# Kernel optimization log

Measured on AMD Instinct MI355X. Metric: run time of the kernel, lower is better.

## Reference

```python
import jax, jax.numpy as jnp
import numpy as np

N = 100000      # nodes
E = 1600000     # edges (before self-loops)
D = 14          # node_dim
H = 64          # hidden_dim
HEADS = 2
C = H // HEADS  # per-head channels = 32
NEG_SLOPE = 0.2 # GATv2Conv default


def setup_inputs() -> dict:
    key = jax.random.key(0)
    ks = jax.random.split(key, 32)
    p = lambda k, shape, s=0.05: (jax.random.normal(k, shape, jnp.float32) * s)
    inp = {
        'node_features': jax.random.normal(ks[0], (N, D), jnp.float32),
        'edge_index': jax.random.randint(ks[1], (2, E), 0, N, jnp.int32),
        # node_proj
        'proj_W': p(ks[2], (D, H)), 'proj_b': p(ks[3], (H,)),
        # GATv2 layer 1 (W_l for source msgs, W_r for target query)
        'g1_Wl': p(ks[4], (H, H)), 'g1_Wr': p(ks[5], (H, H)),
        'g1_att': p(ks[6], (HEADS, C)), 'g1_b': p(ks[7], (H,)),
        # GATv2 layer 2
        'g2_Wl': p(ks[8], (H, H)), 'g2_Wr': p(ks[9], (H, H)),
        'g2_att': p(ks[10], (HEADS, C)), 'g2_b': p(ks[11], (H,)),
        # LayerNorms
        'ln1_g': jnp.ones((H,), jnp.float32), 'ln1_b': jnp.zeros((H,), jnp.float32),
        'ln2_g': jnp.ones((H,), jnp.float32), 'ln2_b': jnp.zeros((H,), jnp.float32),
        # GRU (single step, h0=0). Gate order r,z,n like torch.
        'gru_Wi': p(ks[12], (H, 3 * H)), 'gru_Wh': p(ks[13], (H, 3 * H)),
        'gru_bi': p(ks[14], (3 * H,)), 'gru_bh': p(ks[15], (3 * H,)),
        # heads
        'hu_W': p(ks[16], (H, 1)), 'hu_b': p(ks[17], (1,)),
        'hf_W': p(ks[18], (H, 1)), 'hf_b': p(ks[19], (1,)),
        'ho_W': p(ks[20], (H, 1)), 'ho_b': p(ks[21], (1,)),
        'hc_W': p(ks[22], (H, 1)), 'hc_b': p(ks[23], (1,)),
    }
    return inp


def _layer_norm(x, g, b, eps=1e-5):
    mu = jnp.mean(x, axis=-1, keepdims=True)
    var = jnp.var(x, axis=-1, keepdims=True)
    return (x - mu) * jax.lax.rsqrt(var + eps) * g + b


def _gatv2(x, src, dst, Wl, Wr, att, b):
    n = x.shape[0]
    xl = (x @ Wl).reshape(n, HEADS, C)   # source messages
    xr = (x @ Wr).reshape(n, HEADS, C)   # target queries
    e = jax.nn.leaky_relu(xl[src] + xr[dst], NEG_SLOPE)       # [E', HEADS, C]
    s = jnp.einsum('ehc,hc->eh', e, att)                       # [E', HEADS]
    m = jax.ops.segment_max(s, dst, num_segments=n)            # segment softmax
    ex = jnp.exp(s - m[dst])
    den = jax.ops.segment_sum(ex, dst, num_segments=n)
    alpha = ex / (den[dst] + 1e-16)
    out = jax.ops.segment_sum(alpha[:, :, None] * xl[src], dst, num_segments=n)
    return out.reshape(n, H) + b


def reference(node_features, edge_index, proj_W, proj_b,
              g1_Wl, g1_Wr, g1_att, g1_b,
              g2_Wl, g2_Wr, g2_att, g2_b,
              ln1_g, ln1_b, ln2_g, ln2_b,
              gru_Wi, gru_Wh, gru_bi, gru_bh,
              hu_W, hu_b, hf_W, hf_b, ho_W, ho_b, hc_W, hc_b):
    n = node_features.shape[0]
    # add self-loops (PyG GATv2Conv default)
    loops = jnp.arange(n, dtype=edge_index.dtype)
    src = jnp.concatenate([edge_index[0], loops])
    dst = jnp.concatenate([edge_index[1], loops])

    x = node_features @ proj_W + proj_b
    x = jax.nn.elu(_gatv2(x, src, dst, g1_Wl, g1_Wr, g1_att, g1_b))
    x = _layer_norm(x, ln1_g, ln1_b)
    x = jax.nn.elu(_gatv2(x, src, dst, g2_Wl, g2_Wr, g2_att, g2_b))
    x = _layer_norm(x, ln2_g, ln2_b)

    # single-step GRU, h0 = 0 (gate order r, z, n as in torch)
    gi = x @ gru_Wi + gru_bi
    gi_r, gi_z, gi_n = jnp.split(gi, 3, axis=-1)
    bh_r, bh_z, bh_n = jnp.split(gru_bh, 3)
    r = jax.nn.sigmoid(gi_r + bh_r)
    z = jax.nn.sigmoid(gi_z + bh_z)
    nn_ = jnp.tanh(gi_n + r * bh_n)
    x = (1.0 - z) * nn_  # h' = (1-z)*n + z*h0, h0=0

    utilisation = jax.nn.sigmoid(x @ hu_W + hu_b)
    feasibility = jax.nn.sigmoid(x @ hf_W + hf_b)
    overtime = jax.nn.relu(x @ ho_W + ho_b)
    confidence = jax.nn.sigmoid(x @ hc_W + hc_b)
    return (utilisation, feasibility, overtime, confidence)
```

## Files before the change

### kernel.cpp

```cpp
#include <hip/hip_runtime.h>

#define NDIM 14
#define HDIM 64
#define NB 512
#define EPB 16
#define GSTR 72

typedef __attribute__((ext_vector_type(8))) _Float16 half8;
typedef __attribute__((ext_vector_type(2))) __fp16 fp16x2;
typedef __attribute__((ext_vector_type(4))) float f32x4;

static __device__ __forceinline__ float sigmoidf_(float x) { return 1.f / (1.f + __expf(-x)); }
static __device__ __forceinline__ float lrelu_(float x) { return x > 0.f ? x : 0.2f * x; }

static __device__ __forceinline__ float readlane_f(float x, int lane) {
  return __int_as_float(__builtin_amdgcn_readlane(__float_as_int(x), lane));
}

template <int CTRL>
static __device__ __forceinline__ float dpp_add_f(float x) {
  int v = __builtin_amdgcn_update_dpp(0, __float_as_int(x), CTRL, 0xF, 0xF, true);
  return x + __int_as_float(v);
}

static __device__ __forceinline__ float reduce16(float p) {
  p = dpp_add_f<0xB1>(p);
  p = dpp_add_f<0x4E>(p);
  p = dpp_add_f<0x141>(p);
  p = dpp_add_f<0x140>(p);
  return p;
}
static __device__ __forceinline__ float head_reduce32(float p) {
  p = reduce16(p);
  p += __int_as_float(__builtin_amdgcn_ds_swizzle(__float_as_int(p), 0x401F));
  return p;
}
static __device__ __forceinline__ float full_reduce64(float p) {
  p = head_reduce32(p);
  p += __shfl_xor(p, 32, 64);
  return p;
}

static __device__ __forceinline__ unsigned pk_add(unsigned a, unsigned b) {
  unsigned d; asm("v_pk_add_f16 %0, %1, %2" : "=v"(d) : "v"(a), "v"(b)); return d;
}
static __device__ __forceinline__ unsigned pk_mul(unsigned a, unsigned b) {
  unsigned d; asm("v_pk_mul_f16 %0, %1, %2" : "=v"(d) : "v"(a), "v"(b)); return d;
}
static __device__ __forceinline__ unsigned pk_max(unsigned a, unsigned b) {
  unsigned d; asm("v_pk_max_f16 %0, %1, %2" : "=v"(d) : "v"(a), "v"(b)); return d;
}
static __device__ __forceinline__ unsigned cvt_pk_u(float a, float b) {
  fp16x2 h = __builtin_amdgcn_cvt_pkrtz(a, b);
  unsigned u; __builtin_memcpy(&u, &h, 4); return u;
}
static __device__ __forceinline__ fp16x2 as_h2(unsigned u) {
  fp16x2 h; __builtin_memcpy(&h, &u, 4); return h;
}
static __device__ __forceinline__ float cvt_lo(unsigned u) {
  float r; asm("v_cvt_f32_f16 %0, %1" : "=v"(r) : "v"(u)); return r;
}
template <int CTRL>
static __device__ __forceinline__ unsigned pk_dpp_add(unsigned x) {
  unsigned v = (unsigned)__builtin_amdgcn_update_dpp(0, (int)x, CTRL, 0xF, 0xF, true);
  return pk_add(x, v);
}
static __device__ __forceinline__ unsigned pk_reduce32(unsigned p) {
  p = pk_dpp_add<0xB1>(p);
  p = pk_dpp_add<0x4E>(p);
  p = pk_dpp_add<0x141>(p);
  p = pk_dpp_add<0x140>(p);
  p = pk_add(p, (unsigned)__builtin_amdgcn_ds_swizzle((int)p, 0x401F));
  return p;
}

__global__ void __launch_bounds__(256) k_bin(const int* __restrict__ ei,
                      unsigned* __restrict__ pairs, int* __restrict__ bucket_cur,
                      int E, int bsh) {
  __shared__ int h[NB];
  __shared__ int gb[NB];
  int t = threadIdx.x;
  for (int i = t; i < NB; i += 256) h[i] = 0;
  __syncthreads();
  int c0 = blockIdx.x * (256 * EPB);
  unsigned pr[EPB];
  int br[EPB];
  unsigned lmask = (1u << bsh) - 1u;
#pragma unroll
  for (int i = 0; i < EPB; ++i) {
    int e = c0 + t + i * 256;
    if (e < E) {
      int s = ei[e], d = ei[E + e];
      int b = d >> bsh;
      int r = atomicAdd(&h[b], 1);
      pr[i] = (((unsigned)d & lmask) << 17) | (unsigned)s;
      br[i] = b | (r << 9);
    } else br[i] = -1;
  }
  __syncthreads();
  for (int i = t; i < NB; i += 256)
    if (h[i]) gb[i] = atomicAdd(&bucket_cur[i], h[i]);
  __syncthreads();
#pragma unroll
  for (int i = 0; i < EPB; ++i) {
    if (br[i] >= 0) pairs[gb[br[i] & (NB - 1)] + (br[i] >> 9)] = pr[i];
  }
}

__global__ void __launch_bounds__(256) k_csr(const unsigned* __restrict__ pairs,
                      const int* __restrict__ bcur_final, int* __restrict__ row_off,
                      int* __restrict__ deg, int* __restrict__ csr_src,
                      int N, int bsh, int cap) {
  __shared__ int h[1024];
  __shared__ int cu[1024];
  __shared__ int wtot[4];
  int b = blockIdx.x;
  int node0 = b << bsh;
  int range = 1 << bsh;
  int nr = N - node0; if (nr > range) nr = range;
  if (nr <= 0) return;
  int e0 = b * cap, e1 = bcur_final[b];
  int tid = threadIdx.x;
  for (int i = tid; i < range; i += 256) h[i] = 0;
  __syncthreads();
  for (int e = e0 + tid; e < e1; e += 256)
    atomicAdd(&h[pairs[e] >> 17], 1);
  __syncthreads();
  if (range == 256) {
    int lane = tid & 63, wid = tid >> 6;
    int v = (tid < nr) ? h[tid] : 0;
    int x = v;
#pragma unroll
    for (int m = 1; m <= 32; m <<= 1) {
      int t2 = __shfl_up(x, m, 64);
      if (lane >= m) x += t2;
    }
    if (lane == 63) wtot[wid] = x;
    __syncthreads();
    int woff = 0;
#pragma unroll
    for (int w = 0; w < 4; ++w) woff += (w < wid) ? wtot[w] : 0;
    int excl = woff + x - v;
    if (tid < nr) {
      row_off[node0 + tid] = e0 + excl;
      deg[node0 + tid] = v;
      cu[tid] = excl;
    }
  } else {
    if (tid == 0) {
      int acc = 0;
      for (int i = 0; i < nr; ++i) {
        row_off[node0 + i] = e0 + acc;
        deg[node0 + i] = h[i];
        cu[i] = acc;
        acc += h[i];
      }
    }
  }
  __syncthreads();
  for (int e = e0 + tid; e < e1; e += 256) {
    unsigned pk = pairs[e];
    int dl = (int)(pk >> 17);
    int s = (int)(pk & 0x1FFFFu);
    int p = atomicAdd(&cu[dl], 1);
    csr_src[e0 + p] = s;
  }
}

__global__ void k_wprep(const float* __restrict__ projW, const float* __restrict__ projB,
                        const float* __restrict__ Wl1, const float* __restrict__ Wr1,
                        const float* __restrict__ Wi, const float* __restrict__ Wl2,
                        const float* __restrict__ Wr2,
                        float* __restrict__ Wfl, float* __restrict__ Wfr,
                        float* __restrict__ bfl, float* __restrict__ bfr,
                        _Float16* __restrict__ Wt, _Float16* __restrict__ Wb,
                        int* __restrict__ bcur, int cap) {
  int blk = blockIdx.x;
  if (blk < 4) {
    int t = blk * 256 + threadIdx.x;
    int total = (NDIM + 1) * HDIM;
    if (t >= total) return;
    int r = t / HDIM, c = t % HDIM;
    float al = 0.f, ar = 0.f;
    if (r < NDIM) {
      for (int k = 0; k < HDIM; ++k) {
        float w = projW[r * HDIM + k];
        al += w * Wl1[k * HDIM + c];
        ar += w * Wr1[k * HDIM + c];
      }
      Wfl[r * HDIM + c] = al;
      Wfr[r * HDIM + c] = ar;
    } else {
      for (int k = 0; k < HDIM; ++k) {
        float w = projB[k];
        al += w * Wl1[k * HDIM + c];
        ar += w * Wr1[k * HDIM + c];
      }
      bfl[c] = al;
      bfr[c] = ar;
    }
  } else if (blk < 52) {
    int t = (blk - 4) * 256 + threadIdx.x;
    if (t >= 192 * 64) return;
    int col = t / 64, row = t % 64;
    Wt[col * GSTR + row] = (_Float16)Wi[row * 192 + col];
  } else if (blk < 84) {
    int t = (blk - 52) * 256 + threadIdx.x;
    if (t >= 128 * 64) return;
    int col = t >> 6, row = t & 63;
    float v = (col < 64) ? Wl2[row * 64 + col] : Wr2[row * 64 + (col - 64)];
    Wb[col * GSTR + row] = (_Float16)v;
  } else {
    int i = (blk - 84) * 256 + threadIdx.x;
    if (i < NB) bcur[i] = i * cap;
  }
}

__global__ void k1_xlxr(const float* __restrict__ nf, const float* __restrict__ Wfl,
                        const float* __restrict__ Wfr, const float* __restrict__ bfl,
                        const float* __restrict__ bfr, _Float16* __restrict__ XL16,
                        _Float16* __restrict__ XR16, int N) {
  int n = blockIdx.x * (blockDim.x >> 6) + (threadIdx.x >> 6);
  int j = threadIdx.x & 63;
  if (n >= N) return;
  float nfv = (j < NDIM) ? nf[n * NDIM + j] : 0.f;
  float al = bfl[j], ar = bfr[j];
#pragma unroll
  for (int k = 0; k < NDIM; ++k) {
    float xk = readlane_f(nfv, k);
    al += xk * Wfl[k * HDIM + j];
    ar += xk * Wfr[k * HDIM + j];
  }
  XL16[n * HDIM + j] = (_Float16)al;
  XR16[n * HDIM + j] = (_Float16)ar;
}

__global__ void k_agg(const int* __restrict__ csr_src, const int* __restrict__ row_off,
                      const int* __restrict__ deg, const _Float16* __restrict__ XL16,
                      const _Float16* __restrict__ XR16, const float* __restrict__ att,
                      const float* __restrict__ gb, const float* __restrict__ lng,
                      const float* __restrict__ lnb, float* __restrict__ Y, int N) {
  int n = blockIdx.x * (blockDim.x >> 6) + (threadIdx.x >> 6);
  int j = threadIdx.x & 63;
  if (n >= N) return;
  float xr = (float)XR16[(size_t)n * HDIM + j];
  float attv = att[j];
  unsigned xr_pk  = cvt_pk_u(xr, xr);
  unsigned att_pk = cvt_pk_u(attv, attv);
  unsigned c02_pk = 0x32663266u;
  fp16x2 one_pk = as_h2(0x3C003C00u);
  const unsigned short* XLu = (const unsigned short*)XL16;
  unsigned ju = (unsigned)j;

  float xl = (float)XL16[(size_t)n * HDIM + j];
  float p = head_reduce32(lrelu_(xl + xr) * attv);
  float ex = __expf(p);
  float acc0 = ex * xl, acc1 = 0.f;
  float den0 = ex, den1 = 0.f;

  int base = row_off[n], cnt = deg[n];
  for (int c0 = 0; c0 < cnt; c0 += 64) {
    int m_ = cnt - c0; if (m_ > 64) m_ = 64;
    int sidx = (j < m_) ? csr_src[base + c0 + j] : 0;
    int npairs = m_ >> 1;
    int pp = 0;
    for (; pp + 8 <= npairs; pp += 8) {
      unsigned x[8];
#pragma unroll
      for (int u = 0; u < 8; ++u) {
        int sa = __builtin_amdgcn_readlane(sidx, 2 * (pp + u));
        int sb = __builtin_amdgcn_readlane(sidx, 2 * (pp + u) + 1);
        unsigned ua = XLu[((unsigned)sa << 6) + ju];
        unsigned ub = XLu[((unsigned)sb << 6) + ju];
        x[u] = __builtin_amdgcn_perm(ub, ua, 0x05040100u);
      }
#pragma unroll
      for (int u = 0; u < 8; ++u) {
        unsigned t = pk_add(x[u], xr_pk);
        unsigned lr = pk_max(t, pk_mul(t, c02_pk));
        unsigned sc = pk_mul(lr, att_pk);
        sc = pk_reduce32(sc);
        float s_a = cvt_lo(sc), s_b = cvt_lo(sc >> 16);
        float e_a = __expf(s_a), e_b = __expf(s_b);
        fp16x2 exk = __builtin_amdgcn_cvt_pkrtz(e_a, e_b);
        if (u & 1) {
          acc1 = __builtin_amdgcn_fdot2(as_h2(x[u]), exk, acc1, false);
          den1 = __builtin_amdgcn_fdot2(exk, one_pk, den1, false);
        } else {
          acc0 = __builtin_amdgcn_fdot2(as_h2(x[u]), exk, acc0, false);
          den0 = __builtin_amdgcn_fdot2(exk, one_pk, den0, false);
        }
      }
    }
    for (; pp < npairs; ++pp) {
      int sa = __builtin_amdgcn_readlane(sidx, 2 * pp);
      int sb = __builtin_amdgcn_readlane(sidx, 2 * pp + 1);
      unsigned ua = XLu[((unsigned)sa << 6) + ju];
      unsigned ub = XLu[((unsigned)sb << 6) + ju];
      unsigned xu = __builtin_amdgcn_perm(ub, ua, 0x05040100u);
      unsigned t = pk_add(xu, xr_pk);
      unsigned lr = pk_max(t, pk_mul(t, c02_pk));
      unsigned sc = pk_mul(lr, att_pk);
      sc = pk_reduce32(sc);
      float s_a = cvt_lo(sc), s_b = cvt_lo(sc >> 16);
      float e_a = __expf(s_a), e_b = __expf(s_b);
      fp16x2 exk = __builtin_amdgcn_cvt_pkrtz(e_a, e_b);
      acc0 = __builtin_amdgcn_fdot2(as_h2(xu), exk, acc0, false);
      den0 = __builtin_amdgcn_fdot2(exk, one_pk, den0, false);
    }
    if (m_ & 1) {
      int s = __builtin_amdgcn_readlane(sidx, m_ - 1);
      float xls = (float)XL16[(size_t)s * HDIM + j];
      float pq = head_reduce32(lrelu_(xls + xr) * attv);
      float ee = __expf(pq);
      acc0 += ee * xls;
      den0 += ee;
    }
  }

  float acc = acc0 + acc1;
  float den = den0 + den1;
  float y = acc / (den + 1e-16f) + gb[j];
  y = y > 0.f ? y : __expf(y) - 1.f;
  float mu = full_reduce64(y) * (1.f / 64.f);
  float d = y - mu;
  float var = full_reduce64(d * d) * (1.f / 64.f);
  Y[n * HDIM + j] = d * rsqrtf(var + 1e-5f) * lng[j] + lnb[j];
}

__global__ void __launch_bounds__(256) k3_mfma(const float* __restrict__ Y,
                      const _Float16* __restrict__ Wb, _Float16* __restrict__ XL16,
                      _Float16* __restrict__ XR16, int N) {
  __shared__ _Float16 W[128 * GSTR];
  for (int i = threadIdx.x; i < 128 * GSTR / 8; i += 256)
    ((int4*)W)[i] = ((const int4*)Wb)[i];
  __syncthreads();
  int wave = blockIdx.x * 4 + (threadIdx.x >> 6);
  int nwaves = gridDim.x * 4;
  int lane = threadIdx.x & 63;
  int c = lane & 15, q = lane >> 4;
  for (int n0 = wave * 16; n0 < N; n0 += nwaves * 16) {
    bool okrow = (n0 + c) < N;
    const float* yrow = Y + (size_t)(n0 + c) * HDIM + q * 8;
    float4 v0 = {0,0,0,0}, v1 = {0,0,0,0}, v2 = {0,0,0,0}, v3 = {0,0,0,0};
    if (okrow) {
      v0 = *(const float4*)(yrow);
      v1 = *(const float4*)(yrow + 4);
      v2 = *(const float4*)(yrow + 32);
      v3 = *(const float4*)(yrow + 36);
    }
    half8 a0, a1;
    a0[0]=(_Float16)v0.x; a0[1]=(_Float16)v0.y; a0[2]=(_Float16)v0.z; a0[3]=(_Float16)v0.w;
    a0[4]=(_Float16)v1.x; a0[5]=(_Float16)v1.y; a0[6]=(_Float16)v1.z; a0[7]=(_Float16)v1.w;
    a1[0]=(_Float16)v2.x; a1[1]=(_Float16)v2.y; a1[2]=(_Float16)v2.z; a1[3]=(_Float16)v2.w;
    a1[4]=(_Float16)v3.x; a1[5]=(_Float16)v3.y; a1[6]=(_Float16)v3.z; a1[7]=(_Float16)v3.w;

    f32x4 acc[8];
#pragma unroll
    for (int t = 0; t < 8; ++t) acc[t] = (f32x4){0.f, 0.f, 0.f, 0.f};
#pragma unroll
    for (int t = 0; t < 8; ++t) {
      half8 b0 = *(const half8*)(&W[(t * 16 + c) * GSTR + q * 8]);
      half8 b1 = *(const half8*)(&W[(t * 16 + c) * GSTR + 32 + q * 8]);
      acc[t] = __builtin_amdgcn_mfma_f32_16x16x32_f16(a0, b0, acc[t], 0, 0, 0);
      acc[t] = __builtin_amdgcn_mfma_f32_16x16x32_f16(a1, b1, acc[t], 0, 0, 0);
    }
#pragma unroll
    for (int t = 0; t < 4; ++t) {
#pragma unroll
      for (int i = 0; i < 4; ++i) {
        int n = n0 + q * 4 + i;
        if (n < N) {
          XL16[(size_t)n * HDIM + t * 16 + c] = (_Float16)acc[t][i];
          XR16[(size_t)n * HDIM + t * 16 + c] = (_Float16)acc[t + 4][i];
        }
      }
    }
  }
}

__global__ void __launch_bounds__(256) k5_gru_mfma(const float* __restrict__ Y,
                       const _Float16* __restrict__ Wt,
                       const float* __restrict__ bi, const float* __restrict__ bh,
                       const float* __restrict__ huW, const float* __restrict__ hub,
                       const float* __restrict__ hfW, const float* __restrict__ hfb,
                       const float* __restrict__ hoW, const float* __restrict__ hob,
                       const float* __restrict__ hcW, const float* __restrict__ hcb,
                       float* __restrict__ out, int N) {
  __shared__ _Float16 W[192 * GSTR];
  __shared__ float BS[192];
  __shared__ float BHN[64];
  for (int i = threadIdx.x; i < 192 * GSTR / 8; i += 256)
    ((int4*)W)[i] = ((const int4*)Wt)[i];
  for (int i = threadIdx.x; i < 192; i += 256) BS[i] = bi[i] + (i < 128 ? bh[i] : 0.f);
  for (int i = threadIdx.x; i < 64; i += 256) BHN[i] = bh[128 + i];
  __syncthreads();

  int wave = blockIdx.x * 4 + (threadIdx.x >> 6);
  int nwaves = gridDim.x * 4;
  int lane = threadIdx.x & 63;
  int c = lane & 15, q = lane >> 4;

  float hu_[4], hf_[4], ho_[4], hc_[4];
#pragma unroll
  for (int t = 0; t < 4; ++t) {
    hu_[t] = huW[t * 16 + c];
    hf_[t] = hfW[t * 16 + c];
    ho_[t] = hoW[t * 16 + c];
    hc_[t] = hcW[t * 16 + c];
  }
  float hub0 = hub[0], hfb0 = hfb[0], hob0 = hob[0], hcb0 = hcb[0];

  for (int n0 = wave * 16; n0 < N; n0 += nwaves * 16) {
    bool okrow = (n0 + c) < N;
    const float* yrow = Y + (size_t)(n0 + c) * HDIM + q * 8;
    float4 v0 = {0,0,0,0}, v1 = {0,0,0,0}, v2 = {0,0,0,0}, v3 = {0,0,0,0};
    if (okrow) {
      v0 = *(const float4*)(yrow);
      v1 = *(const float4*)(yrow + 4);
      v2 = *(const float4*)(yrow + 32);
      v3 = *(const float4*)(yrow + 36);
    }
    half8 a0, a1;
    a0[0]=(_Float16)v0.x; a0[1]=(_Float16)v0.y; a0[2]=(_Float16)v0.z; a0[3]=(_Float16)v0.w;
    a0[4]=(_Float16)v1.x; a0[5]=(_Float16)v1.y; a0[6]=(_Float16)v1.z; a0[7]=(_Float16)v1.w;
    a1[0]=(_Float16)v2.x; a1[1]=(_Float16)v2.y; a1[2]=(_Float16)v2.z; a1[3]=(_Float16)v2.w;
    a1[4]=(_Float16)v3.x; a1[5]=(_Float16)v3.y; a1[6]=(_Float16)v3.z; a1[7]=(_Float16)v3.w;

    f32x4 acc[12];
#pragma unroll
    for (int t = 0; t < 12; ++t) acc[t] = (f32x4){0.f, 0.f, 0.f, 0.f};
#pragma unroll
    for (int t = 0; t < 12; ++t) {
      half8 b0 = *(const half8*)(&W[(t * 16 + c) * GSTR + q * 8]);
      half8 b1 = *(const half8*)(&W[(t * 16 + c) * GSTR + 32 + q * 8]);
      acc[t] = __builtin_amdgcn_mfma_f32_16x16x32_f16(a0, b0, acc[t], 0, 0, 0);
      acc[t] = __builtin_amdgcn_mfma_f32_16x16x32_f16(a1, b1, acc[t], 0, 0, 0);
    }

    float hv[4][4];
#pragma unroll
    for (int t = 0; t < 4; ++t) {
      int cr = t * 16 + c;
      float bsr = BS[cr], bsz = BS[64 + cr], bsn = BS[128 + cr], bhn = BHN[cr];
#pragma unroll
      for (int i = 0; i < 4; ++i) {
        float r = sigmoidf_(acc[t][i] + bsr);
        float z = sigmoidf_(acc[t + 4][i] + bsz);
        float nn = tanhf(acc[t + 8][i] + bsn + r * bhn);
        hv[t][i] = (1.f - z) * nn;
      }
    }
#pragma unroll
    for (int i = 0; i < 4; ++i) {
      float pu = 0.f, pf = 0.f, po = 0.f, pc = 0.f;
#pragma unroll
      for (int t = 0; t < 4; ++t) {
        pu += hv[t][i] * hu_[t];
        pf += hv[t][i] * hf_[t];
        po += hv[t][i] * ho_[t];
        pc += hv[t][i] * hc_[t];
      }
      pu = reduce16(pu); pf = reduce16(pf); po = reduce16(po); pc = reduce16(pc);
      int n = n0 + q * 4 + i;
      if (n < N) {
        if (c == 0) out[n]         = sigmoidf_(pu + hub0);
        if (c == 1) out[N + n]     = sigmoidf_(pf + hfb0);
        if (c == 2) out[2 * N + n] = fmaxf(po + hob0, 0.f);
        if (c == 3) out[3 * N + n] = sigmoidf_(pc + hcb0);
      }
    }
  }
}

extern "C" void kernel_launch(void* const* d_in, const int* in_sizes, int n_in,
                              void* d_out, int out_size, void* d_ws, size_t ws_size,
                              hipStream_t stream) {
  const float* nf    = (const float*)d_in[0];
  const int*   ei    = (const int*)d_in[1];
  const float* projW = (const float*)d_in[2];
  const float* projB = (const float*)d_in[3];
  const float* g1Wl  = (const float*)d_in[4];
  const float* g1Wr  = (const float*)d_in[5];
  const float* g1att = (const float*)d_in[6];
  const float* g1b   = (const float*)d_in[7];
  const float* g2Wl  = (const float*)d_in[8];
  const float* g2Wr  = (const float*)d_in[9];
  const float* g2att = (const float*)d_in[10];
  const float* g2b   = (const float*)d_in[11];
  const float* ln1g  = (const float*)d_in[12];
  const float* ln1b  = (const float*)d_in[13];
  const float* ln2g  = (const float*)d_in[14];
  const float* ln2b  = (const float*)d_in[15];
  const float* gruWi = (const float*)d_in[16];
  const float* gruBi = (const float*)d_in[18];
  const float* gruBh = (const float*)d_in[19];
  const float* huW = (const float*)d_in[20];
  const float* hub = (const float*)d_in[21];
  const float* hfW = (const float*)d_in[22];
  const float* hfb = (const float*)d_in[23];
  const float* hoW = (const float*)d_in[24];
  const float* hob = (const float*)d_in[25];
  const float* hcW = (const float*)d_in[26];
  const float* hcb = (const float*)d_in[27];
  float* out = (float*)d_out;

  const int N = in_sizes[0] / NDIM;
  const int E = in_sizes[1] / 2;
  int bsh = 8;
  while (((N - 1) >> bsh) >= NB) ++bsh;
  const int nbu = (N + (1 << bsh) - 1) >> bsh;
  const int cap = (E + nbu - 1) / nbu + 768;

  char* ws = (char*)d_ws;
  size_t off = 0;
  auto carve = [&](size_t bytes) { void* p = ws + off; off += (bytes + 255) & ~size_t(255); return p; };
  _Float16*  XL16    = (_Float16*)carve(sizeof(_Float16) * N * HDIM);
  _Float16*  XR16    = (_Float16*)carve(sizeof(_Float16) * N * HDIM);
  float*     Y       = (float*)carve(sizeof(float) * N * HDIM);
  unsigned*  pairs   = (unsigned*)carve(sizeof(unsigned) * (size_t)nbu * cap);
  int*       csr_src = (int*)carve(sizeof(int) * (size_t)nbu * cap);
  int*       deg     = (int*)carve(sizeof(int) * N);
  int*       row_off = (int*)carve(sizeof(int) * N);
  int*       bcur    = (int*)carve(sizeof(int) * NB);
  float*     Wfl     = (float*)carve(sizeof(float) * NDIM * HDIM);
  float*     Wfr     = (float*)carve(sizeof(float) * NDIM * HDIM);
  float*     bfl     = (float*)carve(sizeof(float) * HDIM);
  float*     bfr     = (float*)carve(sizeof(float) * HDIM);
  _Float16*  Wt      = (_Float16*)carve(sizeof(_Float16) * 192 * GSTR);
  _Float16*  Wb      = (_Float16*)carve(sizeof(_Float16) * 128 * GSTR);

  const int BLK = 256;
  dim3 b(BLK);
  dim3 gridWaveN((N + 3) / 4);
  dim3 gridBin((E + BLK * EPB - 1) / (BLK * EPB));

  k_wprep<<<dim3(86), b, 0, stream>>>(projW, projB, g1Wl, g1Wr, gruWi, g2Wl, g2Wr,
                                      Wfl, Wfr, bfl, bfr, Wt, Wb, bcur, cap);

  k_bin<<<gridBin, b, 0, stream>>>(ei, pairs, bcur, E, bsh);
  k_csr<<<dim3(nbu), b, 0, stream>>>(pairs, bcur, row_off, deg, csr_src, N, bsh, cap);

  k1_xlxr<<<gridWaveN, b, 0, stream>>>(nf, Wfl, Wfr, bfl, bfr, XL16, XR16, N);
  k_agg<<<gridWaveN, b, 0, stream>>>(csr_src, row_off, deg, XL16, XR16, g1att, g1b, ln1g, ln1b, Y, N);
  k3_mfma<<<dim3(800), b, 0, stream>>>(Y, Wb, XL16, XR16, N);
  k_agg<<<gridWaveN, b, 0, stream>>>(csr_src, row_off, deg, XL16, XR16, g2att, g2b, ln2g, ln2b, Y, N);
  k5_gru_mfma<<<dim3(800), b, 0, stream>>>(Y, Wt, gruBi, gruBh,
                                           huW, hub, hfW, hfb, hoW, hob, hcW, hcb, out, N);
}
```

Before: 363.0 us.

## Merge prep kernels into binning/CSR launches and store LayerNorm output as fp16

```diff
diff --git a/kernel.cpp b/kernel.cpp
--- a/kernel.cpp
+++ b/kernel.cpp
@@ -74,12 +74,58 @@
   return p;
 }
 
-__global__ void __launch_bounds__(256) k_bin(const int* __restrict__ ei,
+__global__ void __launch_bounds__(256) k_bin_wprep(const int* __restrict__ ei,
                       unsigned* __restrict__ pairs, int* __restrict__ bucket_cur,
-                      int E, int bsh) {
+                      int E, int bsh, int cap, int nBin,
+                      const float* __restrict__ projW, const float* __restrict__ projB,
+                      const float* __restrict__ Wl1, const float* __restrict__ Wr1,
+                      const float* __restrict__ Wi, const float* __restrict__ Wl2,
+                      const float* __restrict__ Wr2,
+                      float* __restrict__ Wfl, float* __restrict__ Wfr,
+                      float* __restrict__ bfl, float* __restrict__ bfr,
+                      _Float16* __restrict__ Wt, _Float16* __restrict__ Wb) {
   __shared__ int h[NB];
   __shared__ int gb[NB];
   int t = threadIdx.x;
+  if ((int)blockIdx.x >= nBin) {
+    int blk = blockIdx.x - nBin;
+    if (blk < 4) {
+      int tt = blk * 256 + t;
+      int total = (NDIM + 1) * HDIM;
+      if (tt >= total) return;
+      int r = tt / HDIM, c = tt % HDIM;
+      float al = 0.f, ar = 0.f;
+      if (r < NDIM) {
+        for (int k = 0; k < HDIM; ++k) {
+          float w = projW[r * HDIM + k];
+          al += w * Wl1[k * HDIM + c];
+          ar += w * Wr1[k * HDIM + c];
+        }
+        Wfl[r * HDIM + c] = al;
+        Wfr[r * HDIM + c] = ar;
+      } else {
+        for (int k = 0; k < HDIM; ++k) {
+          float w = projB[k];
+          al += w * Wl1[k * HDIM + c];
+          ar += w * Wr1[k * HDIM + c];
+        }
+        bfl[c] = al;
+        bfr[c] = ar;
+      }
+    } else if (blk < 52) {
+      int tt = (blk - 4) * 256 + t;
+      if (tt >= 192 * 64) return;
+      int col = tt / 64, row = tt % 64;
+      Wt[col * GSTR + row] = (_Float16)Wi[row * 192 + col];
+    } else {
+      int tt = (blk - 52) * 256 + t;
+      if (tt >= 128 * 64) return;
+      int col = tt >> 6, row = tt & 63;
+      float v = (col < 64) ? Wl2[row * 64 + col] : Wr2[row * 64 + (col - 64)];
+      Wb[col * GSTR + row] = (_Float16)v;
+    }
+    return;
+  }
   for (int i = t; i < NB; i += 256) h[i] = 0;
   __syncthreads();
   int c0 = blockIdx.x * (256 * EPB);
@@ -103,24 +149,47 @@
   __syncthreads();
 #pragma unroll
   for (int i = 0; i < EPB; ++i) {
-    if (br[i] >= 0) pairs[gb[br[i] & (NB - 1)] + (br[i] >> 9)] = pr[i];
-  }
-}
-
-__global__ void __launch_bounds__(256) k_csr(const unsigned* __restrict__ pairs,
+    if (br[i] >= 0) {
+      int b = br[i] & (NB - 1);
+      pairs[b * cap + gb[b] + (br[i] >> 9)] = pr[i];
+    }
+  }
+}
+
+__global__ void __launch_bounds__(256) k_csr_k1(const unsigned* __restrict__ pairs,
                       const int* __restrict__ bcur_final, int* __restrict__ row_off,
                       int* __restrict__ deg, int* __restrict__ csr_src,
-                      int N, int bsh, int cap) {
+                      int N, int bsh, int cap, int nbu,
+                      const float* __restrict__ nf, const float* __restrict__ Wfl,
+                      const float* __restrict__ Wfr, const float* __restrict__ bfl,
+                      const float* __restrict__ bfr, _Float16* __restrict__ XL16,
+                      _Float16* __restrict__ XR16) {
   __shared__ int h[1024];
   __shared__ int cu[1024];
   __shared__ int wtot[4];
+  int tid = threadIdx.x;
+  if ((int)blockIdx.x >= nbu) {
+    int n = (blockIdx.x - nbu) * 4 + (tid >> 6);
+    int j = tid & 63;
+    if (n >= N) return;
+    float nfv = (j < NDIM) ? nf[n * NDIM + j] : 0.f;
+    float al = bfl[j], ar = bfr[j];
+#pragma unroll
+    for (int k = 0; k < NDIM; ++k) {
+      float xk = readlane_f(nfv, k);
+      al += xk * Wfl[k * HDIM + j];
+      ar += xk * Wfr[k * HDIM + j];
+    }
+    XL16[n * HDIM + j] = (_Float16)al;
+    XR16[n * HDIM + j] = (_Float16)ar;
+    return;
+  }
   int b = blockIdx.x;
   int node0 = b << bsh;
   int range = 1 << bsh;
   int nr = N - node0; if (nr > range) nr = range;
   if (nr <= 0) return;
-  int e0 = b * cap, e1 = bcur_final[b];
-  int tid = threadIdx.x;
+  int e0 = b * cap, e1 = e0 + bcur_final[b];
   for (int i = tid; i < range; i += 256) h[i] = 0;
   __syncthreads();
   for (int e = e0 + tid; e < e1; e += 256)
@@ -167,79 +236,11 @@
   }
 }
 
-__global__ void k_wprep(const float* __restrict__ projW, const float* __restrict__ projB,
-                        const float* __restrict__ Wl1, const float* __restrict__ Wr1,
-                        const float* __restrict__ Wi, const float* __restrict__ Wl2,
-                        const float* __restrict__ Wr2,
-                        float* __restrict__ Wfl, float* __restrict__ Wfr,
-                        float* __restrict__ bfl, float* __restrict__ bfr,
-                        _Float16* __restrict__ Wt, _Float16* __restrict__ Wb,
-                        int* __restrict__ bcur, int cap) {
-  int blk = blockIdx.x;
-  if (blk < 4) {
-    int t = blk * 256 + threadIdx.x;
-    int total = (NDIM + 1) * HDIM;
-    if (t >= total) return;
-    int r = t / HDIM, c = t % HDIM;
-    float al = 0.f, ar = 0.f;
-    if (r < NDIM) {
-      for (int k = 0; k < HDIM; ++k) {
-        float w = projW[r * HDIM + k];
-        al += w * Wl1[k * HDIM + c];
-        ar += w * Wr1[k * HDIM + c];
-      }
-      Wfl[r * HDIM + c] = al;
-      Wfr[r * HDIM + c] = ar;
-    } else {
-      for (int k = 0; k < HDIM; ++k) {
-        float w = projB[k];
-        al += w * Wl1[k * HDIM + c];
-        ar += w * Wr1[k * HDIM + c];
-      }
-      bfl[c] = al;
-      bfr[c] = ar;
-    }
-  } else if (blk < 52) {
-    int t = (blk - 4) * 256 + threadIdx.x;
-    if (t >= 192 * 64) return;
-    int col = t / 64, row = t % 64;
-    Wt[col * GSTR + row] = (_Float16)Wi[row * 192 + col];
-  } else if (blk < 84) {
-    int t = (blk - 52) * 256 + threadIdx.x;
-    if (t >= 128 * 64) return;
-    int col = t >> 6, row = t & 63;
-    float v = (col < 64) ? Wl2[row * 64 + col] : Wr2[row * 64 + (col - 64)];
-    Wb[col * GSTR + row] = (_Float16)v;
-  } else {
-    int i = (blk - 84) * 256 + threadIdx.x;
-    if (i < NB) bcur[i] = i * cap;
-  }
-}
-
-__global__ void k1_xlxr(const float* __restrict__ nf, const float* __restrict__ Wfl,
-                        const float* __restrict__ Wfr, const float* __restrict__ bfl,
-                        const float* __restrict__ bfr, _Float16* __restrict__ XL16,
-                        _Float16* __restrict__ XR16, int N) {
-  int n = blockIdx.x * (blockDim.x >> 6) + (threadIdx.x >> 6);
-  int j = threadIdx.x & 63;
-  if (n >= N) return;
-  float nfv = (j < NDIM) ? nf[n * NDIM + j] : 0.f;
-  float al = bfl[j], ar = bfr[j];
-#pragma unroll
-  for (int k = 0; k < NDIM; ++k) {
-    float xk = readlane_f(nfv, k);
-    al += xk * Wfl[k * HDIM + j];
-    ar += xk * Wfr[k * HDIM + j];
-  }
-  XL16[n * HDIM + j] = (_Float16)al;
-  XR16[n * HDIM + j] = (_Float16)ar;
-}
-
 __global__ void k_agg(const int* __restrict__ csr_src, const int* __restrict__ row_off,
                       const int* __restrict__ deg, const _Float16* __restrict__ XL16,
                       const _Float16* __restrict__ XR16, const float* __restrict__ att,
                       const float* __restrict__ gb, const float* __restrict__ lng,
-                      const float* __restrict__ lnb, float* __restrict__ Y, int N) {
+                      const float* __restrict__ lnb, _Float16* __restrict__ Y16, int N) {
   int n = blockIdx.x * (blockDim.x >> 6) + (threadIdx.x >> 6);
   int j = threadIdx.x & 63;
   if (n >= N) return;
@@ -325,10 +326,10 @@
   float mu = full_reduce64(y) * (1.f / 64.f);
   float d = y - mu;
   float var = full_reduce64(d * d) * (1.f / 64.f);
-  Y[n * HDIM + j] = d * rsqrtf(var + 1e-5f) * lng[j] + lnb[j];
-}
-
-__global__ void __launch_bounds__(256) k3_mfma(const float* __restrict__ Y,
+  Y16[(size_t)n * HDIM + j] = (_Float16)(d * rsqrtf(var + 1e-5f) * lng[j] + lnb[j]);
+}
+
+__global__ void __launch_bounds__(256) k3_mfma(const _Float16* __restrict__ Y16,
                       const _Float16* __restrict__ Wb, _Float16* __restrict__ XL16,
                       _Float16* __restrict__ XR16, int N) {
   __shared__ _Float16 W[128 * GSTR];
@@ -341,19 +342,12 @@
   int c = lane & 15, q = lane >> 4;
   for (int n0 = wave * 16; n0 < N; n0 += nwaves * 16) {
     bool okrow = (n0 + c) < N;
-    const float* yrow = Y + (size_t)(n0 + c) * HDIM + q * 8;
-    float4 v0 = {0,0,0,0}, v1 = {0,0,0,0}, v2 = {0,0,0,0}, v3 = {0,0,0,0};
+    const _Float16* yrow = Y16 + (size_t)(n0 + c) * HDIM + q * 8;
+    half8 a0 = {0, 0, 0, 0, 0, 0, 0, 0}, a1 = {0, 0, 0, 0, 0, 0, 0, 0};
     if (okrow) {
-      v0 = *(const float4*)(yrow);
-      v1 = *(const float4*)(yrow + 4);
-      v2 = *(const float4*)(yrow + 32);
-      v3 = *(const float4*)(yrow + 36);
-    }
-    half8 a0, a1;
-    a0[0]=(_Float16)v0.x; a0[1]=(_Float16)v0.y; a0[2]=(_Float16)v0.z; a0[3]=(_Float16)v0.w;
-    a0[4]=(_Float16)v1.x; a0[5]=(_Float16)v1.y; a0[6]=(_Float16)v1.z; a0[7]=(_Float16)v1.w;
-    a1[0]=(_Float16)v2.x; a1[1]=(_Float16)v2.y; a1[2]=(_Float16)v2.z; a1[3]=(_Float16)v2.w;
-    a1[4]=(_Float16)v3.x; a1[5]=(_Float16)v3.y; a1[6]=(_Float16)v3.z; a1[7]=(_Float16)v3.w;
+      a0 = *(const half8*)(yrow);
+      a1 = *(const half8*)(yrow + 32);
+    }
 
     f32x4 acc[8];
 #pragma unroll
@@ -379,7 +373,7 @@
   }
 }
 
-__global__ void __launch_bounds__(256) k5_gru_mfma(const float* __restrict__ Y,
+__global__ void __launch_bounds__(256) k5_gru_mfma(const _Float16* __restrict__ Y16,
                        const _Float16* __restrict__ Wt,
                        const float* __restrict__ bi, const float* __restrict__ bh,
                        const float* __restrict__ huW, const float* __restrict__ hub,
@@ -413,19 +407,12 @@
 
   for (int n0 = wave * 16; n0 < N; n0 += nwaves * 16) {
     bool okrow = (n0 + c) < N;
-    const float* yrow = Y + (size_t)(n0 + c) * HDIM + q * 8;
-    float4 v0 = {0,0,0,0}, v1 = {0,0,0,0}, v2 = {0,0,0,0}, v3 = {0,0,0,0};
+    const _Float16* yrow = Y16 + (size_t)(n0 + c) * HDIM + q * 8;
+    half8 a0 = {0, 0, 0, 0, 0, 0, 0, 0}, a1 = {0, 0, 0, 0, 0, 0, 0, 0};
     if (okrow) {
-      v0 = *(const float4*)(yrow);
-      v1 = *(const float4*)(yrow + 4);
-      v2 = *(const float4*)(yrow + 32);
-      v3 = *(const float4*)(yrow + 36);
-    }
-    half8 a0, a1;
-    a0[0]=(_Float16)v0.x; a0[1]=(_Float16)v0.y; a0[2]=(_Float16)v0.z; a0[3]=(_Float16)v0.w;
-    a0[4]=(_Float16)v1.x; a0[5]=(_Float16)v1.y; a0[6]=(_Float16)v1.z; a0[7]=(_Float16)v1.w;
-    a1[0]=(_Float16)v2.x; a1[1]=(_Float16)v2.y; a1[2]=(_Float16)v2.z; a1[3]=(_Float16)v2.w;
-    a1[4]=(_Float16)v3.x; a1[5]=(_Float16)v3.y; a1[6]=(_Float16)v3.z; a1[7]=(_Float16)v3.w;
+      a0 = *(const half8*)(yrow);
+      a1 = *(const half8*)(yrow + 32);
+    }
 
     f32x4 acc[12];
 #pragma unroll
@@ -517,7 +504,7 @@
   auto carve = [&](size_t bytes) { void* p = ws + off; off += (bytes + 255) & ~size_t(255); return p; };
   _Float16*  XL16    = (_Float16*)carve(sizeof(_Float16) * N * HDIM);
   _Float16*  XR16    = (_Float16*)carve(sizeof(_Float16) * N * HDIM);
-  float*     Y       = (float*)carve(sizeof(float) * N * HDIM);
+  _Float16*  Y16     = (_Float16*)carve(sizeof(_Float16) * N * HDIM);
   unsigned*  pairs   = (unsigned*)carve(sizeof(unsigned) * (size_t)nbu * cap);
   int*       csr_src = (int*)carve(sizeof(int) * (size_t)nbu * cap);
   int*       deg     = (int*)carve(sizeof(int) * N);
@@ -533,18 +520,18 @@
   const int BLK = 256;
   dim3 b(BLK);
   dim3 gridWaveN((N + 3) / 4);
-  dim3 gridBin((E + BLK * EPB - 1) / (BLK * EPB));
-
-  k_wprep<<<dim3(86), b, 0, stream>>>(projW, projB, g1Wl, g1Wr, gruWi, g2Wl, g2Wr,
-                                      Wfl, Wfr, bfl, bfr, Wt, Wb, bcur, cap);
-
-  k_bin<<<gridBin, b, 0, stream>>>(ei, pairs, bcur, E, bsh);
-  k_csr<<<dim3(nbu), b, 0, stream>>>(pairs, bcur, row_off, deg, csr_src, N, bsh, cap);
-
-  k1_xlxr<<<gridWaveN, b, 0, stream>>>(nf, Wfl, Wfr, bfl, bfr, XL16, XR16, N);
-  k_agg<<<gridWaveN, b, 0, stream>>>(csr_src, row_off, deg, XL16, XR16, g1att, g1b, ln1g, ln1b, Y, N);
-  k3_mfma<<<dim3(800), b, 0, stream>>>(Y, Wb, XL16, XR16, N);
-  k_agg<<<gridWaveN, b, 0, stream>>>(csr_src, row_off, deg, XL16, XR16, g2att, g2b, ln2g, ln2b, Y, N);
-  k5_gru_mfma<<<dim3(800), b, 0, stream>>>(Y, Wt, gruBi, gruBh,
+  const int nBin = (E + BLK * EPB - 1) / (BLK * EPB);
+
+  (void)hipMemsetAsync(bcur, 0, sizeof(int) * NB, stream);
+  k_bin_wprep<<<dim3(nBin + 84), b, 0, stream>>>(ei, pairs, bcur, E, bsh, cap, nBin,
+                                                 projW, projB, g1Wl, g1Wr, gruWi, g2Wl, g2Wr,
+                                                 Wfl, Wfr, bfl, bfr, Wt, Wb);
+  k_csr_k1<<<dim3(nbu + (N + 3) / 4), b, 0, stream>>>(pairs, bcur, row_off, deg, csr_src,
+                                                      N, bsh, cap, nbu,
+                                                      nf, Wfl, Wfr, bfl, bfr, XL16, XR16);
+  k_agg<<<gridWaveN, b, 0, stream>>>(csr_src, row_off, deg, XL16, XR16, g1att, g1b, ln1g, ln1b, Y16, N);
+  k3_mfma<<<dim3(800), b, 0, stream>>>(Y16, Wb, XL16, XR16, N);
+  k_agg<<<gridWaveN, b, 0, stream>>>(csr_src, row_off, deg, XL16, XR16, g2att, g2b, ln2g, ln2b, Y16, N);
+  k5_gru_mfma<<<dim3(800), b, 0, stream>>>(Y16, Wt, gruBi, gruBh,
                                            huW, hub, hfW, hfb, hoW, hob, hcW, hcb, out, N);
 }
```

Measured after the change: 345.7 us. 4.8% less time.
